# Performance work log

Measured on AMD Instinct MI355X. Metric: run time of the kernel, lower is better.

## Reference

```python
import jax, jax.numpy as jnp
import numpy as np

N_HEAD = 16
MODEL_DIM = 1024
HEAD_DIM = MODEL_DIM // N_HEAD


def setup_inputs() -> dict:
    key = jax.random.key(0)
    ks = jax.random.split(key, 12)
    B, S, D = 2, 2048, MODEL_DIM
    scale = 1.0 / np.sqrt(D)
    inp = {
        'q': jax.random.normal(ks[0], (B, S, D), jnp.float32),
        'k': jax.random.normal(ks[1], (B, S, D), jnp.float32),
        'v': jax.random.normal(ks[2], (B, S, D), jnp.float32),
        'mask': jax.random.randint(ks[3], (B, 1, S, S), 0, 2).astype(bool),
        'wq': jax.random.normal(ks[4], (D, D), jnp.float32) * scale,
        'bq': jnp.zeros((D,), jnp.float32),
        'wk': jax.random.normal(ks[5], (D, D), jnp.float32) * scale,
        'bk': jnp.zeros((D,), jnp.float32),
        'wv': jax.random.normal(ks[6], (D, D), jnp.float32) * scale,
        'bv': jnp.zeros((D,), jnp.float32),
        'wo': jax.random.normal(ks[7], (D, D), jnp.float32) * scale,
        'bo': jnp.zeros((D,), jnp.float32),
        'ln_gamma': jnp.ones((D,), jnp.float32),
        'ln_beta': jnp.zeros((D,), jnp.float32),
    }
    return inp


def _split_heads(x):
    B, S, _ = x.shape
    return x.reshape(B, S, N_HEAD, HEAD_DIM).transpose(0, 2, 1, 3)  # [B,H,S,hd]


def reference(q, k, v, mask, wq, bq, wk, bk, wv, bv, wo, bo, ln_gamma, ln_beta):
    residual = q
    qh = _split_heads(q @ wq + bq)
    kh = _split_heads(k @ wk + bk)
    vh = _split_heads(v @ wv + bv)
    dk = jnp.asarray(HEAD_DIM, jnp.float32)
    score = jnp.einsum('bhqd,bhkd->bhqk', qh, kh) / (jnp.sqrt(dk) + 1e-8)
    score = jnp.where(mask, -jnp.inf, score)
    attn = jax.nn.softmax(score, axis=-1)  # [B,H,S,S]
    ctx = jnp.einsum('bhqk,bhkd->bhqd', attn, vh)
    B, H, S, hd = ctx.shape
    ctx = ctx.transpose(0, 2, 1, 3).reshape(B, S, H * hd)
    out = ctx @ wo + bo  # dropout is identity in eval
    x = residual + out
    mu = jnp.mean(x, axis=-1, keepdims=True)
    var = jnp.var(x, axis=-1, keepdims=True)
    xn = (x - mu) / jnp.sqrt(var + 1e-5)
    return xn * ln_gamma + ln_beta
```

## Files before the change

kernel.cpp:

```cpp
#include <hip/hip_runtime.h>
#include <hip/hip_fp16.h>
#include <math.h>


typedef _Float16 half8 __attribute__((ext_vector_type(8)));
typedef _Float16 half4v __attribute__((ext_vector_type(4)));
typedef float f32x4 __attribute__((ext_vector_type(4)));

#define MFMA16(a, b, c) __builtin_amdgcn_mfma_f32_16x16x32_f16((a), (b), (c), 0, 0, 0)

static __device__ __forceinline__ half8 cvt8(float4 a, float4 b) {
    half8 h;
    h[0] = (_Float16)a.x; h[1] = (_Float16)a.y; h[2] = (_Float16)a.z; h[3] = (_Float16)a.w;
    h[4] = (_Float16)b.x; h[5] = (_Float16)b.y; h[6] = (_Float16)b.z; h[7] = (_Float16)b.w;
    return h;
}

__global__ void mask_detect_kernel(const unsigned int* __restrict__ m, int* __restrict__ flag) {
    __shared__ int any;
    if (threadIdx.x == 0) any = 0;
    __syncthreads();
    unsigned v = 0;
#pragma unroll
    for (int i = 0; i < 8; ++i) v |= m[threadIdx.x + i * 256];
    if (v > 1u) atomicOr(&any, 1);
    __syncthreads();
    if (threadIdx.x == 0) *flag = any;
}

__global__ void mask_bias_kernel(const void* __restrict__ mask, const int* __restrict__ flag,
                                 _Float16* __restrict__ mb) {
    const int i = (blockIdx.x * 256 + threadIdx.x) * 4;
    const bool bytemode = (*flag != 0);
    int v0, v1, v2, v3;
    if (bytemode) {
        const unsigned int w = *(const unsigned int*)((const unsigned char*)mask + i);
        v0 = w & 0xff; v1 = (w >> 8) & 0xff; v2 = (w >> 16) & 0xff; v3 = (w >> 24) & 0xff;
    } else {
        const int4 w = *(const int4*)((const int*)mask + i);
        v0 = w.x; v1 = w.y; v2 = w.z; v3 = w.w;
    }
    const _Float16 NEG = (_Float16)(-60000.0f);
    const _Float16 ZER = (_Float16)(0.0f);
    half4v o = { v0 ? NEG : ZER, v1 ? NEG : ZER, v2 ? NEG : ZER, v3 ? NEG : ZER };
    *(half4v*)(mb + i) = o;
}

__global__ void wtrans_kernel(const float* __restrict__ W, _Float16* __restrict__ Wt) {
    __shared__ float t[32][33];
    const int tx = threadIdx.x, ty = threadIdx.y;
    const int n0 = blockIdx.x * 32, k0 = blockIdx.y * 32;
#pragma unroll
    for (int i = 0; i < 4; ++i)
        t[ty + i * 8][tx] = W[(size_t)(k0 + ty + i * 8) * 1024 + n0 + tx];
    __syncthreads();
#pragma unroll
    for (int i = 0; i < 4; ++i)
        Wt[(size_t)(n0 + ty + i * 8) * 1024 + k0 + tx] = (_Float16)t[tx][ty + i * 8];
}

__global__ void vtrans_kernel(const _Float16* __restrict__ Vh, _Float16* __restrict__ Vt) {
    __shared__ _Float16 t[32][33];
    const int tx = threadIdx.x, ty = threadIdx.y;
    const int d0 = blockIdx.x * 32, s0 = blockIdx.y * 32, bh = blockIdx.z;
    const _Float16* src = Vh + (size_t)bh * 2048 * 64;
    _Float16* dst = Vt + (size_t)bh * 64 * 2048;
#pragma unroll
    for (int i = 0; i < 4; ++i)
        t[ty + i * 8][tx] = src[(size_t)(s0 + ty + i * 8) * 64 + d0 + tx];
    __syncthreads();
#pragma unroll
    for (int i = 0; i < 4; ++i)
        dst[(size_t)(d0 + ty + i * 8) * 2048 + s0 + tx] = t[tx][ty + i * 8];
}

__global__ __launch_bounds__(256) void gemm_qkv_kernel(
    const float* __restrict__ Aq, const float* __restrict__ Ak, const float* __restrict__ Av,
    const _Float16* __restrict__ Btbase,
    const float* __restrict__ bq, const float* __restrict__ bk, const float* __restrict__ bv,
    _Float16* __restrict__ Hbase) {
    constexpr int K = 1024;
    const int z = blockIdx.z;
    const float* A = (z == 0) ? Aq : ((z == 1) ? Ak : Av);
    const _Float16* Bt = Btbase + (size_t)z * 1024 * 1024;
    const float* bias = (z == 0) ? bq : ((z == 1) ? bk : bv);
    _Float16* outh = Hbase + (size_t)z * 32 * 2048 * 64;

    __shared__ __align__(16) _Float16 As[128 * 32];
    __shared__ __align__(16) _Float16 Bs[128 * 32];
    const int tid = threadIdx.x;
    const int mBase = blockIdx.x * 128, nBase = blockIdx.y * 128;
    const int r0 = tid >> 2, c0 = (tid & 3) * 8;
    const float* gA = A + (size_t)(mBase + r0) * K + c0;
    const _Float16* gB = Bt + (size_t)(nBase + r0) * K + c0;
    const int lane = tid & 63, wid = tid >> 6;
    const int wm = (wid >> 1) * 64, wn = (wid & 1) * 64;
    const int fr = lane & 15, fg = lane >> 4;

    f32x4 acc[4][4] = {};
    float4 a00 = *(const float4*)(gA);
    float4 a01 = *(const float4*)(gA + 4);
    float4 a10 = *(const float4*)(gA + 64 * K);
    float4 a11 = *(const float4*)(gA + 64 * K + 4);
    half8 rb0 = *(const half8*)(gB);
    half8 rb1 = *(const half8*)(gB + 64 * K);
    for (int kt = 0; kt < K / 32; ++kt) {
        __syncthreads();
        *(half8*)&As[tid * 8] = cvt8(a00, a01);
        *(half8*)&As[tid * 8 + 2048] = cvt8(a10, a11);
        *(half8*)&Bs[tid * 8] = rb0;
        *(half8*)&Bs[tid * 8 + 2048] = rb1;
        __syncthreads();
        if (kt + 1 < K / 32) {
            const int k1 = (kt + 1) * 32;
            a00 = *(const float4*)(gA + k1);
            a01 = *(const float4*)(gA + k1 + 4);
            a10 = *(const float4*)(gA + 64 * K + k1);
            a11 = *(const float4*)(gA + 64 * K + k1 + 4);
            rb0 = *(const half8*)(gB + k1);
            rb1 = *(const half8*)(gB + 64 * K + k1);
        }
        half8 af[4], bfv[4];
#pragma unroll
        for (int i = 0; i < 4; ++i) af[i] = *(const half8*)&As[(wm + i * 16 + fr) * 32 + fg * 8];
#pragma unroll
        for (int i = 0; i < 4; ++i) bfv[i] = *(const half8*)&Bs[(wn + i * 16 + fr) * 32 + fg * 8];
#pragma unroll
        for (int mi = 0; mi < 4; ++mi)
#pragma unroll
            for (int ni = 0; ni < 4; ++ni)
                acc[mi][ni] = MFMA16(af[mi], bfv[ni], acc[mi][ni]);
    }
#pragma unroll
    for (int mi = 0; mi < 4; ++mi)
#pragma unroll
        for (int ni = 0; ni < 4; ++ni)
#pragma unroll
            for (int j = 0; j < 4; ++j) {
                const int row = mBase + wm + mi * 16 + fg * 4 + j;
                const int col = nBase + wn + ni * 16 + fr;
                const float v = acc[mi][ni][j] + bias[col];
                const int b = row >> 11, s = row & 2047, h = col >> 6, d = col & 63;
                outh[(((size_t)(b * 16 + h) * 2048) + s) * 64 + d] = (_Float16)v;
            }
}

__global__ __launch_bounds__(256) void gemm_out_kernel(
    const _Float16* __restrict__ A, const _Float16* __restrict__ Bt,
    const float* __restrict__ bias, const float* __restrict__ resid,
    float* __restrict__ outf) {
    constexpr int K = 1024;
    __shared__ __align__(16) _Float16 As[128 * 32];
    __shared__ __align__(16) _Float16 Bs[128 * 32];
    const int tid = threadIdx.x;
    const int mBase = blockIdx.x * 128, nBase = blockIdx.y * 128;
    const int r0 = tid >> 2, c0 = (tid & 3) * 8;
    const _Float16* gA = A + (size_t)(mBase + r0) * K + c0;
    const _Float16* gB = Bt + (size_t)(nBase + r0) * K + c0;
    const int lane = tid & 63, wid = tid >> 6;
    const int wm = (wid >> 1) * 64, wn = (wid & 1) * 64;
    const int fr = lane & 15, fg = lane >> 4;

    f32x4 acc[4][4] = {};
    half8 ra0 = *(const half8*)(gA);
    half8 ra1 = *(const half8*)(gA + 64 * K);
    half8 rb0 = *(const half8*)(gB);
    half8 rb1 = *(const half8*)(gB + 64 * K);
    for (int kt = 0; kt < K / 32; ++kt) {
        __syncthreads();
        *(half8*)&As[tid * 8] = ra0;
        *(half8*)&As[tid * 8 + 2048] = ra1;
        *(half8*)&Bs[tid * 8] = rb0;
        *(half8*)&Bs[tid * 8 + 2048] = rb1;
        __syncthreads();
        if (kt + 1 < K / 32) {
            const int k1 = (kt + 1) * 32;
            ra0 = *(const half8*)(gA + k1);
            ra1 = *(const half8*)(gA + 64 * K + k1);
            rb0 = *(const half8*)(gB + k1);
            rb1 = *(const half8*)(gB + 64 * K + k1);
        }
        half8 af[4], bfv[4];
#pragma unroll
        for (int i = 0; i < 4; ++i) af[i] = *(const half8*)&As[(wm + i * 16 + fr) * 32 + fg * 8];
#pragma unroll
        for (int i = 0; i < 4; ++i) bfv[i] = *(const half8*)&Bs[(wn + i * 16 + fr) * 32 + fg * 8];
#pragma unroll
        for (int mi = 0; mi < 4; ++mi)
#pragma unroll
            for (int ni = 0; ni < 4; ++ni)
                acc[mi][ni] = MFMA16(af[mi], bfv[ni], acc[mi][ni]);
    }
#pragma unroll
    for (int mi = 0; mi < 4; ++mi)
#pragma unroll
        for (int ni = 0; ni < 4; ++ni)
#pragma unroll
            for (int j = 0; j < 4; ++j) {
                const int row = mBase + wm + mi * 16 + fg * 4 + j;
                const int col = nBase + wn + ni * 16 + fr;
                const size_t idx = (size_t)row * 1024 + col;
                outf[idx] = acc[mi][ni][j] + bias[col] + resid[idx];
            }
}

__global__ __launch_bounds__(256) void attn_kernel(
    const _Float16* __restrict__ Qh, const _Float16* __restrict__ Kh,
    const _Float16* __restrict__ Vt, const _Float16* __restrict__ mb,
    _Float16* __restrict__ ctx) {
    constexpr int S = 2048;
    constexpr int KT = 128;
    __shared__ __align__(16) _Float16 Ks[128][64];
    __shared__ __align__(16) _Float16 Vs[64][128];
    __shared__ __align__(16) _Float16 Pl[4][16][128];
    const int tid = threadIdx.x, lane = tid & 63, wid = tid >> 6;
    const int fr = lane & 15, fg = lane >> 4;
    const int bh = blockIdx.y;
    const int b = bh >> 4, h = bh & 15;
    const int q0 = blockIdx.x * 64 + wid * 16;
    const int q = q0 + fr;
    const _Float16* Qp = Qh + (size_t)bh * S * 64;
    const _Float16* Kp = Kh + (size_t)bh * S * 64;
    const _Float16* Vp = Vt + (size_t)bh * 64 * S;
    const _Float16* mrow = mb + ((size_t)b * S + q) * S + fg * 32;

    half8 qf0 = *(const half8*)(Qp + (size_t)q * 64 + fg * 8);
    half8 qf1 = *(const half8*)(Qp + (size_t)q * 64 + 32 + fg * 8);
    const _Float16 QSC = (_Float16)0.18033688f;
#pragma unroll
    for (int i = 0; i < 8; ++i) { qf0[i] = qf0[i] * QSC; qf1[i] = qf1[i] * QSC; }
    half8 ones8;
#pragma unroll
    for (int i = 0; i < 8; ++i) ones8[i] = (_Float16)1.0f;

    const int kCol = (tid & 7) * 8;
    const int vCol = (tid & 15) * 8;
    int kTrue[4], kW[4], vRow[4], vW[4];
#pragma unroll
    for (int n = 0; n < 4; ++n) {
        const int p = (tid >> 3) + 32 * n;
        kTrue[n] = ((p & 15) << 3) | (p >> 4);
        kW[n] = p * 64 + (kCol ^ ((p & 7) << 3));
        const int d = (tid >> 4) + 16 * n;
        vRow[n] = d;
        vW[n] = d * 128 + (vCol ^ ((d & 15) << 3));
    }
    const int swzK = (fr & 7) << 3;
    const int swzV = fr << 3;

    f32x4 acc[4] = {};
    f32x4 accl = {};
    float m_r = -1e30f;
    const float TH = 11.5f;

    half8 sK[4], sV[4], mcur[4], mnx[4];
#pragma unroll
    for (int n = 0; n < 4; ++n) {
        sK[n] = *(const half8*)(Kp + (size_t)kTrue[n] * 64 + kCol);
        sV[n] = *(const half8*)(Vp + (size_t)vRow[n] * S + vCol);
        mcur[n] = *(const half8*)(mrow + n * 8);
    }

    _Float16* Pw = &Pl[wid][0][0];

    for (int t = 0; t < 16; ++t) {
        __syncthreads();
#pragma unroll
        for (int n = 0; n < 4; ++n) {
            *(half8*)&Ks[0][kW[n]] = sK[n];
            *(half8*)&Vs[0][vW[n]] = sV[n];
        }
        __syncthreads();

        const int kn = (t < 15) ? (t + 1) * KT : t * KT;
#pragma unroll
        for (int n = 0; n < 4; ++n) {
            sK[n] = *(const half8*)(Kp + (size_t)(kn + kTrue[n]) * 64 + kCol);
            sV[n] = *(const half8*)(Vp + (size_t)vRow[n] * S + kn + vCol);
            mnx[n] = *(const half8*)(mrow + kn + n * 8);
        }

        f32x4 tt[8];
#pragma unroll
        for (int s = 0; s < 8; ++s) {
            const int p = s * 16 + fr;
            const half8 ka0 = *(const half8*)&Ks[0][p * 64 + ((fg * 8) ^ swzK)];
            const half8 ka1 = *(const half8*)&Ks[0][p * 64 + ((32 + fg * 8) ^ swzK)];
            f32x4 z = {};
            tt[s] = MFMA16(ka0, qf0, z);
            tt[s] = MFMA16(ka1, qf1, tt[s]);
        }

        float pmax = -1e30f;
#pragma unroll
        for (int s = 0; s < 8; ++s)
#pragma unroll
            for (int j = 0; j < 4; ++j) {
                tt[s][j] += (float)mcur[j][s];
                pmax = fmaxf(pmax, tt[s][j]);
            }
        if (__any(pmax > m_r + TH)) {
            pmax = fmaxf(pmax, __shfl_xor(pmax, 16));
            pmax = fmaxf(pmax, __shfl_xor(pmax, 32));
            const float mnew = fmaxf(m_r, pmax);
            const float scf = exp2f(m_r - mnew);
#pragma unroll
            for (int n = 0; n < 4; ++n)
#pragma unroll
                for (int j = 0; j < 4; ++j) acc[n][j] *= scf;
#pragma unroll
            for (int j = 0; j < 4; ++j) accl[j] *= scf;
            m_r = mnew;
        }
#pragma unroll
        for (int s = 0; s < 8; ++s)
#pragma unroll
            for (int j = 0; j < 4; ++j)
                tt[s][j] = exp2f(tt[s][j] - m_r);

#pragma unroll
        for (int m = 0; m < 4; ++m) {
            half8 w;
#pragma unroll
            for (int e = 0; e < 8; ++e) w[e] = (_Float16)tt[e][m];
            *(half8*)&Pw[fr * 128 + ((fg * 32 + m * 8) ^ swzK)] = w;
        }

#pragma unroll
        for (int c = 0; c < 4; ++c) {
            const half8 pa = *(const half8*)&Pw[fr * 128 + ((c * 32 + fg * 8) ^ swzK)];
            accl = MFMA16(ones8, pa, accl);
#pragma unroll
            for (int n = 0; n < 4; ++n) {
                const int d = n * 16 + fr;
                const half8 vb = *(const half8*)&Vs[0][d * 128 + ((c * 32 + fg * 8) ^ swzV)];
                acc[n] = MFMA16(vb, pa, acc[n]);
            }
        }
#pragma unroll
        for (int n = 0; n < 4; ++n) mcur[n] = mnx[n];
    }

    const float inv = 1.0f / accl[0];
#pragma unroll
    for (int n = 0; n < 4; ++n) {
        half4v o = { (_Float16)(acc[n][0] * inv), (_Float16)(acc[n][1] * inv),
                     (_Float16)(acc[n][2] * inv), (_Float16)(acc[n][3] * inv) };
        *(half4v*)&ctx[((size_t)b * 2048 + q) * 1024 + h * 64 + n * 16 + fg * 4] = o;
    }
}

__global__ __launch_bounds__(256) void ln_kernel(
    const float* __restrict__ y, const float* __restrict__ gamma,
    const float* __restrict__ beta, float* __restrict__ out) {
    const int row = blockIdx.x, tid = threadIdx.x;
    const size_t base = (size_t)row * 1024 + tid * 4;
    const float4 v = *(const float4*)(y + base);
    float s = v.x + v.y + v.z + v.w;
    float ss = v.x * v.x + v.y * v.y + v.z * v.z + v.w * v.w;
#pragma unroll
    for (int o = 1; o < 64; o <<= 1) {
        s += __shfl_xor(s, o, 64);
        ss += __shfl_xor(ss, o, 64);
    }
    __shared__ float red[8];
    const int wid = tid >> 6;
    if ((tid & 63) == 0) { red[wid] = s; red[wid + 4] = ss; }
    __syncthreads();
    s = red[0] + red[1] + red[2] + red[3];
    ss = red[4] + red[5] + red[6] + red[7];
    const float mu = s * (1.0f / 1024.0f);
    const float var = ss * (1.0f / 1024.0f) - mu * mu;
    const float rstd = rsqrtf(var + 1e-5f);
    const float4 g = *(const float4*)(gamma + tid * 4);
    const float4 bt = *(const float4*)(beta + tid * 4);
    float4 o;
    o.x = (v.x - mu) * rstd * g.x + bt.x;
    o.y = (v.y - mu) * rstd * g.y + bt.y;
    o.z = (v.z - mu) * rstd * g.z + bt.z;
    o.w = (v.w - mu) * rstd * g.w + bt.w;
    *(float4*)(out + base) = o;
}

extern "C" void kernel_launch(void* const* d_in, const int* in_sizes, int n_in,
                              void* d_out, int out_size, void* d_ws, size_t ws_size,
                              hipStream_t stream) {
    (void)in_sizes; (void)n_in; (void)out_size; (void)ws_size;
    const float* q     = (const float*)d_in[0];
    const float* k     = (const float*)d_in[1];
    const float* v     = (const float*)d_in[2];
    const void*  mask  = d_in[3];
    const float* wq    = (const float*)d_in[4];
    const float* bq    = (const float*)d_in[5];
    const float* wk    = (const float*)d_in[6];
    const float* bk    = (const float*)d_in[7];
    const float* wv    = (const float*)d_in[8];
    const float* bv    = (const float*)d_in[9];
    const float* wo    = (const float*)d_in[10];
    const float* bo    = (const float*)d_in[11];
    const float* gamma = (const float*)d_in[12];
    const float* beta  = (const float*)d_in[13];

    char* ws = (char*)d_ws;
    constexpr size_t SZ_H = (size_t)4096 * 1024 * 2;
    constexpr size_t SZ_W = (size_t)1024 * 1024 * 2;
    size_t off = 256;
    int* flag = (int*)ws;
    _Float16* wqt = (_Float16*)(ws + off); off += SZ_W;
    _Float16* wkt = (_Float16*)(ws + off); off += SZ_W;
    _Float16* wvt = (_Float16*)(ws + off); off += SZ_W;
    _Float16* wot = (_Float16*)(ws + off); off += SZ_W;
    _Float16* scratchA = (_Float16*)(ws + off); off += SZ_H;
    _Float16* scratchB = (_Float16*)(ws + off); off += SZ_H;
    _Float16* scratchC = (_Float16*)(ws + off); off += SZ_H;
    _Float16* Qh  = (_Float16*)(ws + off); off += SZ_H;
    _Float16* Kh  = (_Float16*)(ws + off); off += SZ_H;
    _Float16* Vh  = (_Float16*)(ws + off); off += SZ_H;
    _Float16* Vt  = (_Float16*)(ws + off); off += SZ_H;
    _Float16* mb  = (_Float16*)(ws + off); off += (size_t)2 * 2048 * 2048 * 2;
    _Float16* ctx = scratchA;
    float*    y   = (float*)scratchB;

    mask_detect_kernel<<<1, 256, 0, stream>>>((const unsigned int*)mask, flag);
    dim3 tb(32, 8);
    wtrans_kernel<<<dim3(32, 32), tb, 0, stream>>>(wq, wqt);
    wtrans_kernel<<<dim3(32, 32), tb, 0, stream>>>(wk, wkt);
    wtrans_kernel<<<dim3(32, 32), tb, 0, stream>>>(wv, wvt);
    wtrans_kernel<<<dim3(32, 32), tb, 0, stream>>>(wo, wot);
    mask_bias_kernel<<<8192, 256, 0, stream>>>(mask, flag, mb);

    gemm_qkv_kernel<<<dim3(32, 8, 3), 256, 0, stream>>>(q, k, v, wqt, bq, bk, bv, Qh);
    vtrans_kernel<<<dim3(2, 64, 32), tb, 0, stream>>>(Vh, Vt);
    attn_kernel<<<dim3(32, 32), 256, 0, stream>>>(Qh, Kh, Vt, mb, ctx);
    gemm_out_kernel<<<dim3(32, 8), 256, 0, stream>>>(ctx, wot, bo, q, y);
    ln_kernel<<<4096, 256, 0, stream>>>(y, gamma, beta, (float*)d_out);
}
```

Baseline: 195.7 us.

## Use multiplicative keep-mask, alias P buffer onto K smem, add MFMA priority

```diff
diff --git a/kernel.cpp b/kernel.cpp
--- a/kernel.cpp
+++ b/kernel.cpp
@@ -28,8 +28,8 @@
     if (threadIdx.x == 0) *flag = any;
 }
 
-__global__ void mask_bias_kernel(const void* __restrict__ mask, const int* __restrict__ flag,
-                                 _Float16* __restrict__ mb) {
+__global__ void mask_keep_kernel(const void* __restrict__ mask, const int* __restrict__ flag,
+                                 _Float16* __restrict__ km) {
     const int i = (blockIdx.x * 256 + threadIdx.x) * 4;
     const bool bytemode = (*flag != 0);
     int v0, v1, v2, v3;
@@ -40,10 +40,10 @@
         const int4 w = *(const int4*)((const int*)mask + i);
         v0 = w.x; v1 = w.y; v2 = w.z; v3 = w.w;
     }
-    const _Float16 NEG = (_Float16)(-60000.0f);
-    const _Float16 ZER = (_Float16)(0.0f);
-    half4v o = { v0 ? NEG : ZER, v1 ? NEG : ZER, v2 ? NEG : ZER, v3 ? NEG : ZER };
-    *(half4v*)(mb + i) = o;
+    const _Float16 ONE = (_Float16)1.0f;
+    const _Float16 ZER = (_Float16)0.0f;
+    half4v o = { v0 ? ZER : ONE, v1 ? ZER : ONE, v2 ? ZER : ONE, v3 ? ZER : ONE };
+    *(half4v*)(km + i) = o;
 }
 
 __global__ void wtrans_kernel(const float* __restrict__ W, _Float16* __restrict__ Wt) {
@@ -204,15 +204,14 @@
             }
 }
 
-__global__ __launch_bounds__(256) void attn_kernel(
+__global__ __launch_bounds__(256, 5) void attn_kernel(
     const _Float16* __restrict__ Qh, const _Float16* __restrict__ Kh,
-    const _Float16* __restrict__ Vt, const _Float16* __restrict__ mb,
+    const _Float16* __restrict__ Vt, const _Float16* __restrict__ km,
     _Float16* __restrict__ ctx) {
     constexpr int S = 2048;
     constexpr int KT = 128;
     __shared__ __align__(16) _Float16 Ks[128][64];
     __shared__ __align__(16) _Float16 Vs[64][128];
-    __shared__ __align__(16) _Float16 Pl[4][16][128];
     const int tid = threadIdx.x, lane = tid & 63, wid = tid >> 6;
     const int fr = lane & 15, fg = lane >> 4;
     const int bh = blockIdx.y;
@@ -222,7 +221,7 @@
     const _Float16* Qp = Qh + (size_t)bh * S * 64;
     const _Float16* Kp = Kh + (size_t)bh * S * 64;
     const _Float16* Vp = Vt + (size_t)bh * 64 * S;
-    const _Float16* mrow = mb + ((size_t)b * S + q) * S + fg * 32;
+    const _Float16* mrow = km + ((size_t)b * S + q) * S + fg * 32;
 
     half8 qf0 = *(const half8*)(Qp + (size_t)q * 64 + fg * 8);
     half8 qf1 = *(const half8*)(Qp + (size_t)q * 64 + 32 + fg * 8);
@@ -261,7 +260,7 @@
         mcur[n] = *(const half8*)(mrow + n * 8);
     }
 
-    _Float16* Pw = &Pl[wid][0][0];
+    _Float16* Pw = &Ks[0][0] + wid * 2048;
 
     for (int t = 0; t < 16; ++t) {
         __syncthreads();
@@ -281,6 +280,7 @@
         }
 
         f32x4 tt[8];
+        __builtin_amdgcn_s_setprio(1);
 #pragma unroll
         for (int s = 0; s < 8; ++s) {
             const int p = s * 16 + fr;
@@ -290,15 +290,14 @@
             tt[s] = MFMA16(ka0, qf0, z);
             tt[s] = MFMA16(ka1, qf1, tt[s]);
         }
+        __builtin_amdgcn_s_setprio(0);
+        __syncthreads();
 
         float pmax = -1e30f;
 #pragma unroll
         for (int s = 0; s < 8; ++s)
 #pragma unroll
-            for (int j = 0; j < 4; ++j) {
-                tt[s][j] += (float)mcur[j][s];
-                pmax = fmaxf(pmax, tt[s][j]);
-            }
+            for (int j = 0; j < 4; ++j) pmax = fmaxf(pmax, tt[s][j]);
         if (__any(pmax > m_r + TH)) {
             pmax = fmaxf(pmax, __shfl_xor(pmax, 16));
             pmax = fmaxf(pmax, __shfl_xor(pmax, 32));
@@ -322,10 +321,15 @@
         for (int m = 0; m < 4; ++m) {
             half8 w;
 #pragma unroll
-            for (int e = 0; e < 8; ++e) w[e] = (_Float16)tt[e][m];
+            for (int a = 0; a < 4; ++a) {
+                auto p2 = __builtin_amdgcn_cvt_pkrtz(tt[2 * a][m], tt[2 * a + 1][m]);
+                w[2 * a] = (_Float16)p2[0]; w[2 * a + 1] = (_Float16)p2[1];
+            }
+            w *= mcur[m];
             *(half8*)&Pw[fr * 128 + ((fg * 32 + m * 8) ^ swzK)] = w;
         }
 
+        __builtin_amdgcn_s_setprio(1);
 #pragma unroll
         for (int c = 0; c < 4; ++c) {
             const half8 pa = *(const half8*)&Pw[fr * 128 + ((c * 32 + fg * 8) ^ swzK)];
@@ -337,6 +341,7 @@
                 acc[n] = MFMA16(vb, pa, acc[n]);
             }
         }
+        __builtin_amdgcn_s_setprio(0);
 #pragma unroll
         for (int n = 0; n < 4; ++n) mcur[n] = mnx[n];
     }
@@ -417,7 +422,7 @@
     _Float16* Kh  = (_Float16*)(ws + off); off += SZ_H;
     _Float16* Vh  = (_Float16*)(ws + off); off += SZ_H;
     _Float16* Vt  = (_Float16*)(ws + off); off += SZ_H;
-    _Float16* mb  = (_Float16*)(ws + off); off += (size_t)2 * 2048 * 2048 * 2;
+    _Float16* km  = (_Float16*)(ws + off); off += (size_t)2 * 2048 * 2048 * 2;
     _Float16* ctx = scratchA;
     float*    y   = (float*)scratchB;
 
@@ -427,11 +432,11 @@
     wtrans_kernel<<<dim3(32, 32), tb, 0, stream>>>(wk, wkt);
     wtrans_kernel<<<dim3(32, 32), tb, 0, stream>>>(wv, wvt);
     wtrans_kernel<<<dim3(32, 32), tb, 0, stream>>>(wo, wot);
-    mask_bias_kernel<<<8192, 256, 0, stream>>>(mask, flag, mb);
+    mask_keep_kernel<<<8192, 256, 0, stream>>>(mask, flag, km);
 
     gemm_qkv_kernel<<<dim3(32, 8, 3), 256, 0, stream>>>(q, k, v, wqt, bq, bk, bv, Qh);
     vtrans_kernel<<<dim3(2, 64, 32), tb, 0, stream>>>(Vh, Vt);
-    attn_kernel<<<dim3(32, 32), 256, 0, stream>>>(Qh, Kh, Vt, mb, ctx);
+    attn_kernel<<<dim3(32, 32), 256, 0, stream>>>(Qh, Kh, Vt, km, ctx);
     gemm_out_kernel<<<dim3(32, 8), 256, 0, stream>>>(ctx, wot, bo, q, y);
     ln_kernel<<<4096, 256, 0, stream>>>(y, gamma, beta, (float*)d_out);
 }
```

Result: slower. 365.1 us (+86.6%).
